# Kernel optimization log

Measured on AMD Instinct MI355X. Metric: run time of the kernel, lower is better.

Reference implementation:

```python
import jax, jax.numpy as jnp
import numpy as np

B, T, W_DIM = 32, 2048, 1024
G, D = 16, 64          # num_groups, input_dim (w = G*D)
MOM = 0.9
TH = 0.5
EPS = 1e-8
TOP_K = 2


def setup_inputs() -> dict:
    key = jax.random.key(0)
    k = jax.random.split(key, 4)
    x = jax.random.normal(k[0], (B, T, W_DIM), dtype=jnp.float32)
    ema = jnp.zeros((W_DIM, W_DIM), dtype=jnp.float32)
    W1 = jax.random.normal(k[1], (G, 16, D), dtype=jnp.float32) * 0.05
    b1 = jnp.zeros((G, 16), dtype=jnp.float32)
    W2 = jax.random.normal(k[2], (G, 1, 16), dtype=jnp.float32) * 0.05
    b2 = jnp.zeros((G, 1), dtype=jnp.float32)
    return {"x": x, "ema": ema, "W1": W1, "b1": b1, "W2": W2, "b2": b2}


def _corr_over_T(x):
    # x: (B, T, w) -> per-batch Pearson corr over the T axis: (B, w, w)
    Tn = x.shape[1]
    c = x - x.mean(axis=1, keepdims=True)
    cov = jnp.einsum('btw,btv->bwv', c, c) / (Tn - 1)
    std = jnp.sqrt(jnp.sum(c * c, axis=1) / (Tn - 1))  # (B, w)
    return jnp.clip(cov / (std[:, :, None] * std[:, None, :] + EPS), -1.0, 1.0)


def reference(x, ema, W1, b1, W2, b2):
    # --- burst-masked EMA update (torch.no_grad) ---
    corr_batch = jax.lax.stop_gradient(_corr_over_T(x))  # (B, w, w)

    def step(e, c):
        mask = jnp.abs(c) > TH
        return jnp.where(mask, MOM * e + (1.0 - MOM) * c, e), None

    ema_new, _ = jax.lax.scan(step, ema, corr_batch)

    # --- split into groups: (B, T, G, D) ---
    Bn, Tn, w = x.shape
    groups = x.reshape(Bn, Tn, G, D)

    # --- per-group correlation score: mean |off-diagonal| of within-group corr ---
    cg = groups - groups.mean(axis=1, keepdims=True)
    cov_g = jnp.einsum('btgd,btge->bgde', cg, cg) / (Tn - 1)        # (B, G, D, D)
    std_g = jnp.sqrt(jnp.sum(cg * cg, axis=1) / (Tn - 1))           # (B, G, D)
    corr_g = jnp.clip(cov_g / (std_g[..., :, None] * std_g[..., None, :] + EPS), -1.0, 1.0)
    absc = jnp.abs(corr_g)
    offdiag = (absc.sum(axis=(-2, -1)) - jnp.einsum('bgdd->bg', absc)) / (D * D - D)
    correlations = offdiag.mean(axis=0)                              # (G,)

    # --- select the 2 least-correlated groups (these get gradients) ---
    _, sel = jax.lax.top_k(-correlations, TOP_K)
    sel_mask = jnp.zeros((G,), dtype=bool).at[sel].set(True)

    # --- per-group expert MLP: D -> 16 -> 1, batched over groups ---
    h = jax.nn.relu(jnp.einsum('btgd,ghd->btgh', groups, W1) + b1)   # (B, T, G, 16)
    o = (jnp.einsum('btgh,goh->btgo', h, W2) + b2)[..., 0]           # (B, T, G)

    # non-selected groups run under no_grad -> stop_gradient on their outputs
    out = jnp.where(sel_mask[None, None, :], o, jax.lax.stop_gradient(o))
    return out, correlations, ema_new
```

## Files before the change

### kernel.cpp

```cpp
#include <hip/hip_runtime.h>
#include <hip/hip_bf16.h>
#include <stdint.h>

#define B_   32
#define T_   2048
#define W_   1024
#define G_   16
#define D_   64
#define LIST_CAP 65536
#define BK   64

typedef __bf16 bf16_t;
typedef __bf16 bf16x8 __attribute__((ext_vector_type(8)));
typedef float  f32x4  __attribute__((ext_vector_type(4)));

#define WS_XT      0ull
#define WS_XT_SZ   (134217728ull)
#define WS_SUM     (WS_XT + WS_XT_SZ)
#define WS_SQ      (WS_SUM + 131072ull)
#define WS_MU      (WS_SQ  + 131072ull)
#define WS_SIG     (WS_MU  + 131072ull)
#define WS_ACCUM   (WS_SIG + 131072ull)
#define WS_LISTCNT (WS_ACCUM + 256ull)
#define WS_LIST    (WS_LISTCNT + 256ull)
#define WS_MASK    (WS_LIST + 1048576ull)
#define WS_DIAG    (WS_MASK + 4194304ull)

__global__ __launch_bounds__(256) void stats_transpose(
    const float* __restrict__ x, bf16_t* __restrict__ xT,
    float* __restrict__ sumb, float* __restrict__ sqb) {
  int b = blockIdx.z, t0 = blockIdx.x * 64, w0 = blockIdx.y * 64;
  __shared__ float tile[64][65];
  __shared__ float rs[64][17], rq[64][17];
  int tid = threadIdx.x;
  int wc = tid & 15, tr = tid >> 4;
  float4 s4 = {0.f, 0.f, 0.f, 0.f}, q4 = {0.f, 0.f, 0.f, 0.f};
  const float4* xp = (const float4*)(x + ((size_t)b * T_ + t0) * W_ + w0);
#pragma unroll
  for (int p = 0; p < 4; ++p) {
    int t = tr + 16 * p;
    float4 v = xp[(size_t)t * 256 + wc];
    s4.x += v.x; s4.y += v.y; s4.z += v.z; s4.w += v.w;
    q4.x += v.x * v.x; q4.y += v.y * v.y; q4.z += v.z * v.z; q4.w += v.w * v.w;
    tile[4 * wc + 0][t] = v.x;
    tile[4 * wc + 1][t] = v.y;
    tile[4 * wc + 2][t] = v.z;
    tile[4 * wc + 3][t] = v.w;
  }
  rs[4 * wc + 0][tr] = s4.x; rs[4 * wc + 1][tr] = s4.y;
  rs[4 * wc + 2][tr] = s4.z; rs[4 * wc + 3][tr] = s4.w;
  rq[4 * wc + 0][tr] = q4.x; rq[4 * wc + 1][tr] = q4.y;
  rq[4 * wc + 2][tr] = q4.z; rq[4 * wc + 3][tr] = q4.w;
  __syncthreads();
  if (tid < 64) {
    float s = 0.f, q = 0.f;
#pragma unroll
    for (int i = 0; i < 16; ++i) { s += rs[tid][i]; q += rq[tid][i]; }
    atomicAdd(&sumb[b * W_ + w0 + tid], s);
    atomicAdd(&sqb[b * W_ + w0 + tid], q);
  }
  int c = tid & 7, wv = tid >> 3;
#pragma unroll
  for (int p = 0; p < 2; ++p) {
    int w = wv + 32 * p;
    const float* src = &tile[w][c * 8];
    bf16x8 o;
#pragma unroll
    for (int k = 0; k < 8; ++k) o[k] = (bf16_t)src[k];
    *(bf16x8*)(xT + ((size_t)b * W_ + w0 + w) * T_ + t0 + c * 8) = o;
  }
}

__global__ void finalize_stats(const float* __restrict__ sumb,
                               const float* __restrict__ sqb,
                               float* __restrict__ mu, float* __restrict__ sig) {
  int idx = blockIdx.x * 256 + threadIdx.x;
  float s = sumb[idx], q = sqb[idx];
  float m = s * (1.0f / 2048.0f);
  float var = (q - s * m) * (1.0f / 2047.0f);
  if (var < 0.f) var = 0.f;
  mu[idx] = m;
  sig[idx] = sqrtf(var);
}

__global__ __launch_bounds__(256) void gram_kernel(
    const bf16_t* __restrict__ xT, const float* __restrict__ mu,
    const float* __restrict__ sig, unsigned int* __restrict__ mask,
    float* __restrict__ diagv, int* __restrict__ listcnt,
    int4* __restrict__ list, float* __restrict__ accum) {
  int id = blockIdx.x;
  int xcd = id & 7;
  int idx = id >> 3;
  int sub = idx / 36;
  int rt  = idx % 36;
  int b = sub * 8 + xcd;
  int r = rt, ti = 0;
  while (r >= 8 - ti) { r -= 8 - ti; ++ti; }
  int tj = ti + r;
  int i0 = ti * 128, j0 = tj * 128;

  const bf16_t* Ag = xT + ((size_t)b * W_ + i0) * T_;
  const bf16_t* Bg = xT + ((size_t)b * W_ + j0) * T_;

  __shared__ __attribute__((aligned(16))) bf16_t As[2][128 * BK];
  __shared__ __attribute__((aligned(16))) bf16_t Bs[2][128 * BK];

  int tid = threadIdx.x;
  int lane = tid & 63, wave = tid >> 6;
  int wm = wave >> 1, wn = wave & 1;

  auto stage = [&](int buf, int k0) {
    bf16_t* Ad = &As[buf][0];
    bf16_t* Bd = &Bs[buf][0];
#pragma unroll
    for (int s = 0; s < 4; ++s) {
      int c = s * 256 + tid;
      int row = c >> 3, slot = c & 7;
      int gslot = slot ^ (row & 7);
      __builtin_amdgcn_global_load_lds(
          (const __attribute__((address_space(1))) void*)(Ag + (size_t)row * T_ + k0 + gslot * 8),
          (__attribute__((address_space(3))) void*)(Ad + c * 8), 16, 0, 0);
      __builtin_amdgcn_global_load_lds(
          (const __attribute__((address_space(1))) void*)(Bg + (size_t)row * T_ + k0 + gslot * 8),
          (__attribute__((address_space(3))) void*)(Bd + c * 8), 16, 0, 0);
    }
  };

  f32x4 zero = {0.f, 0.f, 0.f, 0.f};
  f32x4 acc[4][4];
#pragma unroll
  for (int mi = 0; mi < 4; ++mi)
#pragma unroll
    for (int nj = 0; nj < 4; ++nj) acc[mi][nj] = zero;

  int arow = wm * 64 + (lane & 15);
  int brow = wn * 64 + (lane & 15);
  int q = lane >> 4;

  stage(0, 0);

  const int NT = T_ / BK;
#pragma unroll 1
  for (int kt = 0; kt < NT; ++kt) {
    int cur = kt & 1;
    if (kt + 1 < NT) {
      stage(cur ^ 1, (kt + 1) * BK);
      asm volatile("s_waitcnt vmcnt(8)" ::: "memory");
    } else {
      asm volatile("s_waitcnt vmcnt(0)" ::: "memory");
    }
    __builtin_amdgcn_s_barrier();
    __builtin_amdgcn_sched_barrier(0);

    const bf16_t* Ac = &As[cur][0];
    const bf16_t* Bc = &Bs[cur][0];
#pragma unroll
    for (int s2 = 0; s2 < 2; ++s2) {
      bf16x8 af[4], bfr[4];
#pragma unroll
      for (int mi = 0; mi < 4; ++mi) {
        int row = arow + mi * 16;
        af[mi] = *(const bf16x8*)(Ac + row * BK + ((s2 * 4 + q) ^ (row & 7)) * 8);
      }
#pragma unroll
      for (int nj = 0; nj < 4; ++nj) {
        int row = brow + nj * 16;
        bfr[nj] = *(const bf16x8*)(Bc + row * BK + ((s2 * 4 + q) ^ (row & 7)) * 8);
      }
#pragma unroll
      for (int mi = 0; mi < 4; ++mi)
#pragma unroll
        for (int nj = 0; nj < 4; ++nj)
          acc[mi][nj] = __builtin_amdgcn_mfma_f32_16x16x32_bf16(af[mi], bfr[nj], acc[mi][nj], 0, 0, 0);
    }
    asm volatile("s_waitcnt lgkmcnt(0)" ::: "memory");
    __builtin_amdgcn_sched_barrier(0);
    __builtin_amdgcn_s_barrier();
  }

  const float inv = 1.0f / 2047.0f;
  const float* mub = mu + b * W_;
  const float* sgb = sig + b * W_;
  bool diagquad = (ti == tj) && (wm == wn);
  float gsum = 0.f;

#pragma unroll
  for (int nj = 0; nj < 4; ++nj) {
    int j = j0 + wn * 64 + nj * 16 + (lane & 15);
    float muj = mub[j], sgj = sgb[j];
#pragma unroll
    for (int mi = 0; mi < 4; ++mi) {
#pragma unroll
      for (int rr = 0; rr < 4; ++rr) {
        int i = i0 + wm * 64 + mi * 16 + (lane >> 4) * 4 + rr;
        float cov = (acc[mi][nj][rr] - 2048.0f * mub[i] * muj) * inv;
        float corr = cov / (sgb[i] * sgj + 1e-8f);
        corr = fminf(1.0f, fmaxf(-1.0f, corr));
        if (diagquad && (i != j)) gsum += fabsf(corr);
        if (fabsf(corr) > 0.5f) {
          atomicOr(&mask[i * W_ + j], 1u << b);
          if (i == j) {
            diagv[b * W_ + i] = corr;
          } else {
            int p = atomicAdd(listcnt, 1);
            if (p < LIST_CAP) list[p] = make_int4(b, i, j, __float_as_int(corr));
          }
          if (ti != tj) {
            atomicOr(&mask[j * W_ + i], 1u << b);
            int p = atomicAdd(listcnt, 1);
            if (p < LIST_CAP) list[p] = make_int4(b, j, i, __float_as_int(corr));
          }
        }
      }
    }
  }
  if (diagquad) {
    for (int o = 32; o > 0; o >>= 1) gsum += __shfl_down(gsum, o);
    if (lane == 0) atomicAdd(&accum[ti * 2 + wm], gsum);
  }
}

__global__ void ema_kernel(const float* __restrict__ ema,
                           const unsigned int* __restrict__ mask,
                           const float* __restrict__ diagv,
                           const int* __restrict__ listcnt,
                           const int4* __restrict__ list,
                           float* __restrict__ emaout) {
  int idx = blockIdx.x * 256 + threadIdx.x;
  int i = idx >> 10, j = idx & 1023;
  float e = ema[idx];
  unsigned int m = mask[idx];
  if (m) {
    if (i == j) {
      for (int b = 0; b < 32; ++b)
        if ((m >> b) & 1u) e = 0.9f * e + 0.1f * diagv[b * W_ + i];
    } else {
      int cnt = *listcnt; if (cnt > LIST_CAP) cnt = LIST_CAP;
      for (int b = 0; b < 32; ++b) {
        if ((m >> b) & 1u) {
          for (int k = 0; k < cnt; ++k) {
            int4 t = list[k];
            if (t.x == b && t.y == i && t.z == j) {
              e = 0.9f * e + 0.1f * __int_as_float(t.w);
              break;
            }
          }
        }
      }
    }
  }
  emaout[idx] = e;
}

__global__ void corr_finalize(const float* __restrict__ accum, float* __restrict__ outc) {
  int g = threadIdx.x;
  if (g < 16) outc[g] = accum[g] * (1.0f / (32.0f * 4032.0f));
}

__global__ __launch_bounds__(256) void mlp_kernel(
    const float* __restrict__ x, const float* __restrict__ W1,
    const float* __restrict__ b1, const float* __restrict__ W2,
    const float* __restrict__ b2, float* __restrict__ out) {
  int b = blockIdx.y, t0 = blockIdx.x * 64, gs = blockIdx.z * 4;
  int tid = threadIdx.x;
  int gl = tid & 3, tl = tid >> 2;
  __shared__ __attribute__((aligned(16))) float Wt[4 * 1092 + 16];
  __shared__ float b1s[16 * 4], W2s[16 * 4], b2s[4];
  for (int l = tid; l < 4096; l += 256) {
    int g2 = l >> 10, r = l & 1023;
    int j = r >> 6, d = r & 63;
    Wt[g2 * 1092 + j * 68 + d] = W1[(size_t)(gs + g2) * 1024 + r];
  }
  if (tid < 64) {
    int g2 = tid & 3, j = tid >> 2;
    b1s[j * 4 + g2] = b1[(gs + g2) * 16 + j];
    W2s[j * 4 + g2] = W2[(gs + g2) * 16 + j];
  }
  if (tid < 4) b2s[tid] = b2[gs + tid];
  __syncthreads();

  int g = gs + gl, t = t0 + tl;
  const float4* xp = (const float4*)(x + ((size_t)b * T_ + t) * W_ + g * D_);
  const float* wbase = &Wt[gl * 1092];
  float h[16];
#pragma unroll
  for (int j = 0; j < 16; ++j) h[j] = b1s[j * 4 + gl];
#pragma unroll
  for (int d4 = 0; d4 < 16; ++d4) {
    float4 xv = xp[d4];
#pragma unroll
    for (int j = 0; j < 16; ++j) {
      float4 wv = *(const float4*)(wbase + j * 68 + d4 * 4);
      h[j] += xv.x * wv.x + xv.y * wv.y + xv.z * wv.z + xv.w * wv.w;
    }
  }
  float o = b2s[gl];
#pragma unroll
  for (int j = 0; j < 16; ++j) o += fmaxf(h[j], 0.f) * W2s[j * 4 + gl];
  out[((size_t)b * T_ + t) * 16 + g] = o;
}

extern "C" void kernel_launch(void* const* d_in, const int* in_sizes, int n_in,
                              void* d_out, int out_size, void* d_ws, size_t ws_size,
                              hipStream_t stream) {
  const float* x   = (const float*)d_in[0];
  const float* ema = (const float*)d_in[1];
  const float* W1  = (const float*)d_in[2];
  const float* b1  = (const float*)d_in[3];
  const float* W2  = (const float*)d_in[4];
  const float* b2  = (const float*)d_in[5];

  float* out    = (float*)d_out;
  float* outc   = out + 1048576;
  float* outema = outc + 16;

  char* ws = (char*)d_ws;
  bf16_t* xT        = (bf16_t*)(ws + WS_XT);
  float* sumb       = (float*)(ws + WS_SUM);
  float* sqb        = (float*)(ws + WS_SQ);
  float* mub        = (float*)(ws + WS_MU);
  float* sigb       = (float*)(ws + WS_SIG);
  float* accum      = (float*)(ws + WS_ACCUM);
  int*   listcnt    = (int*)(ws + WS_LISTCNT);
  int4*  list       = (int4*)(ws + WS_LIST);
  unsigned int* msk = (unsigned int*)(ws + WS_MASK);
  float* diagv      = (float*)(ws + WS_DIAG);

  hipMemsetAsync(ws + WS_SUM, 0, 262144, stream);
  hipMemsetAsync(ws + WS_ACCUM, 0, 512, stream);
  hipMemsetAsync(ws + WS_MASK, 0, 4194304, stream);

  stats_transpose<<<dim3(32, 16, 32), 256, 0, stream>>>(x, xT, sumb, sqb);
  finalize_stats<<<128, 256, 0, stream>>>(sumb, sqb, mub, sigb);
  gram_kernel<<<1152, 256, 0, stream>>>(xT, mub, sigb, msk, diagv, listcnt, list, accum);
  ema_kernel<<<4096, 256, 0, stream>>>(ema, msk, diagv, listcnt, list, outema);
  corr_finalize<<<1, 16, 0, stream>>>(accum, outc);
  mlp_kernel<<<dim3(32, 32, 4), 256, 0, stream>>>(x, W1, b1, W2, b2, out);
}
```

Before: 698.7 us.

## Triple-buffer gram K-loop with single barrier; compute four timesteps per MLP thread

The gram kernel moves from a double-buffered BK=64 loop with two barriers per step to a triple-buffered BK=32 loop. It prefetches two stages ahead, adjusts the LDS swizzle for 64-byte rows, and keeps only one barrier per iteration, so global-to-LDS loads overlap MFMA work with less synchronisation. The MLP kernel now has each thread compute four timesteps, which reuses every LDS weight read four times and cuts the grid by 4x. The trade-off is more loop iterations with less MFMA work each in the gram kernel, and higher register pressure in the MLP kernel.

```diff
diff --git a/kernel.cpp b/kernel.cpp
--- a/kernel.cpp
+++ b/kernel.cpp
@@ -8,7 +8,7 @@
 #define G_   16
 #define D_   64
 #define LIST_CAP 65536
-#define BK   64
+#define BK   32
 
 typedef __bf16 bf16_t;
 typedef __bf16 bf16x8 __attribute__((ext_vector_type(8)));
@@ -102,8 +102,8 @@
   const bf16_t* Ag = xT + ((size_t)b * W_ + i0) * T_;
   const bf16_t* Bg = xT + ((size_t)b * W_ + j0) * T_;
 
-  __shared__ __attribute__((aligned(16))) bf16_t As[2][128 * BK];
-  __shared__ __attribute__((aligned(16))) bf16_t Bs[2][128 * BK];
+  __shared__ __attribute__((aligned(16))) bf16_t As[3][128 * BK];
+  __shared__ __attribute__((aligned(16))) bf16_t Bs[3][128 * BK];
 
   int tid = threadIdx.x;
   int lane = tid & 63, wave = tid >> 6;
@@ -113,10 +113,10 @@
     bf16_t* Ad = &As[buf][0];
     bf16_t* Bd = &Bs[buf][0];
 #pragma unroll
-    for (int s = 0; s < 4; ++s) {
+    for (int s = 0; s < 2; ++s) {
       int c = s * 256 + tid;
-      int row = c >> 3, slot = c & 7;
-      int gslot = slot ^ (row & 7);
+      int row = c >> 2, slot = c & 3;
+      int gslot = slot ^ ((row >> 1) & 3);
       __builtin_amdgcn_global_load_lds(
           (const __attribute__((address_space(1))) void*)(Ag + (size_t)row * T_ + k0 + gslot * 8),
           (__attribute__((address_space(3))) void*)(Ad + c * 8), 16, 0, 0);
@@ -138,44 +138,39 @@
   int q = lane >> 4;
 
   stage(0, 0);
+  stage(1, BK);
 
   const int NT = T_ / BK;
 #pragma unroll 1
   for (int kt = 0; kt < NT; ++kt) {
-    int cur = kt & 1;
-    if (kt + 1 < NT) {
-      stage(cur ^ 1, (kt + 1) * BK);
-      asm volatile("s_waitcnt vmcnt(8)" ::: "memory");
+    int cur = kt % 3;
+    if (kt < NT - 1) {
+      asm volatile("s_waitcnt vmcnt(4)" ::: "memory");
     } else {
       asm volatile("s_waitcnt vmcnt(0)" ::: "memory");
     }
     __builtin_amdgcn_s_barrier();
-    __builtin_amdgcn_sched_barrier(0);
 
     const bf16_t* Ac = &As[cur][0];
     const bf16_t* Bc = &Bs[cur][0];
-#pragma unroll
-    for (int s2 = 0; s2 < 2; ++s2) {
-      bf16x8 af[4], bfr[4];
-#pragma unroll
-      for (int mi = 0; mi < 4; ++mi) {
-        int row = arow + mi * 16;
-        af[mi] = *(const bf16x8*)(Ac + row * BK + ((s2 * 4 + q) ^ (row & 7)) * 8);
-      }
-#pragma unroll
-      for (int nj = 0; nj < 4; ++nj) {
-        int row = brow + nj * 16;
-        bfr[nj] = *(const bf16x8*)(Bc + row * BK + ((s2 * 4 + q) ^ (row & 7)) * 8);
-      }
-#pragma unroll
-      for (int mi = 0; mi < 4; ++mi)
-#pragma unroll
-        for (int nj = 0; nj < 4; ++nj)
-          acc[mi][nj] = __builtin_amdgcn_mfma_f32_16x16x32_bf16(af[mi], bfr[nj], acc[mi][nj], 0, 0, 0);
-    }
-    asm volatile("s_waitcnt lgkmcnt(0)" ::: "memory");
-    __builtin_amdgcn_sched_barrier(0);
-    __builtin_amdgcn_s_barrier();
+    bf16x8 af[4], bfr[4];
+#pragma unroll
+    for (int mi = 0; mi < 4; ++mi) {
+      int row = arow + mi * 16;
+      af[mi] = *(const bf16x8*)(Ac + row * BK + (q ^ ((row >> 1) & 3)) * 8);
+    }
+#pragma unroll
+    for (int nj = 0; nj < 4; ++nj) {
+      int row = brow + nj * 16;
+      bfr[nj] = *(const bf16x8*)(Bc + row * BK + (q ^ ((row >> 1) & 3)) * 8);
+    }
+#pragma unroll
+    for (int mi = 0; mi < 4; ++mi)
+#pragma unroll
+      for (int nj = 0; nj < 4; ++nj)
+        acc[mi][nj] = __builtin_amdgcn_mfma_f32_16x16x32_bf16(af[mi], bfr[nj], acc[mi][nj], 0, 0, 0);
+
+    if (kt < NT - 2) stage((kt + 2) % 3, (kt + 2) * BK);
   }
 
   const float inv = 1.0f / 2047.0f;
@@ -261,7 +256,7 @@
     const float* __restrict__ x, const float* __restrict__ W1,
     const float* __restrict__ b1, const float* __restrict__ W2,
     const float* __restrict__ b2, float* __restrict__ out) {
-  int b = blockIdx.y, t0 = blockIdx.x * 64, gs = blockIdx.z * 4;
+  int b = blockIdx.y, t0 = blockIdx.x * 256, gs = blockIdx.z * 4;
   int tid = threadIdx.x;
   int gl = tid & 3, tl = tid >> 2;
   __shared__ __attribute__((aligned(16))) float Wt[4 * 1092 + 16];
@@ -279,25 +274,44 @@
   if (tid < 4) b2s[tid] = b2[gs + tid];
   __syncthreads();
 
-  int g = gs + gl, t = t0 + tl;
-  const float4* xp = (const float4*)(x + ((size_t)b * T_ + t) * W_ + g * D_);
+  int g = gs + gl;
+  const float* xb = x + ((size_t)b * T_ + t0 + tl) * W_ + g * D_;
   const float* wbase = &Wt[gl * 1092];
-  float h[16];
-#pragma unroll
-  for (int j = 0; j < 16; ++j) h[j] = b1s[j * 4 + gl];
+  float h0[16], h1[16], h2[16], h3[16];
+#pragma unroll
+  for (int j = 0; j < 16; ++j) {
+    float bj = b1s[j * 4 + gl];
+    h0[j] = bj; h1[j] = bj; h2[j] = bj; h3[j] = bj;
+  }
 #pragma unroll
   for (int d4 = 0; d4 < 16; ++d4) {
-    float4 xv = xp[d4];
+    float4 x0 = *(const float4*)(xb + 0 * 64 * W_ + d4 * 4);
+    float4 x1 = *(const float4*)(xb + 1 * 64 * W_ + d4 * 4);
+    float4 x2 = *(const float4*)(xb + 2 * 64 * W_ + d4 * 4);
+    float4 x3 = *(const float4*)(xb + 3 * 64 * W_ + d4 * 4);
 #pragma unroll
     for (int j = 0; j < 16; ++j) {
       float4 wv = *(const float4*)(wbase + j * 68 + d4 * 4);
-      h[j] += xv.x * wv.x + xv.y * wv.y + xv.z * wv.z + xv.w * wv.w;
-    }
-  }
-  float o = b2s[gl];
-#pragma unroll
-  for (int j = 0; j < 16; ++j) o += fmaxf(h[j], 0.f) * W2s[j * 4 + gl];
-  out[((size_t)b * T_ + t) * 16 + g] = o;
+      h0[j] += x0.x * wv.x + x0.y * wv.y + x0.z * wv.z + x0.w * wv.w;
+      h1[j] += x1.x * wv.x + x1.y * wv.y + x1.z * wv.z + x1.w * wv.w;
+      h2[j] += x2.x * wv.x + x2.y * wv.y + x2.z * wv.z + x2.w * wv.w;
+      h3[j] += x3.x * wv.x + x3.y * wv.y + x3.z * wv.z + x3.w * wv.w;
+    }
+  }
+  size_t ob = ((size_t)b * T_ + t0 + tl) * 16 + g;
+  float o0 = b2s[gl], o1 = b2s[gl], o2 = b2s[gl], o3 = b2s[gl];
+#pragma unroll
+  for (int j = 0; j < 16; ++j) {
+    float w2 = W2s[j * 4 + gl];
+    o0 += fmaxf(h0[j], 0.f) * w2;
+    o1 += fmaxf(h1[j], 0.f) * w2;
+    o2 += fmaxf(h2[j], 0.f) * w2;
+    o3 += fmaxf(h3[j], 0.f) * w2;
+  }
+  out[ob + 0 * 64 * 16] = o0;
+  out[ob + 1 * 64 * 16] = o1;
+  out[ob + 2 * 64 * 16] = o2;
+  out[ob + 3 * 64 * 16] = o3;
 }
 
 extern "C" void kernel_launch(void* const* d_in, const int* in_sizes, int n_in,
@@ -335,5 +349,5 @@
   gram_kernel<<<1152, 256, 0, stream>>>(xT, mub, sigb, msk, diagv, listcnt, list, accum);
   ema_kernel<<<4096, 256, 0, stream>>>(ema, msk, diagv, listcnt, list, outema);
   corr_finalize<<<1, 16, 0, stream>>>(accum, outc);
-  mlp_kernel<<<dim3(32, 32, 4), 256, 0, stream>>>(x, W1, b1, W2, b2, out);
-}
+  mlp_kernel<<<dim3(8, 32, 4), 256, 0, stream>>>(x, W1, b1, W2, b2, out);
+}
```

Measured after the change: 697.1 us. Within noise of the previous version (-0.2%).
